# Kernel tuning notes

Measured on AMD Instinct MI355X. Metric: run time of the kernel, lower is better.

The kernel has to match this reference:

```python
import jax, jax.numpy as jnp
import numpy as np

D_MODEL = 768; D_REF = 768; N_LAYER = 8
EXPAND = 2; D_STATE = 128; HEADDIM = 64; D_CONV = 4
D_INNER = EXPAND * D_MODEL              # 1536
NHEADS = D_INNER // HEADDIM             # 24
CONV_DIM = D_INNER + 2 * D_STATE        # 1792
D_IN_PROJ = 2 * D_INNER + 2 * D_STATE + NHEADS  # 3352
AH = 8; AD = 64; AINNER = AH * AD       # cross-attn heads/dim
RMS_EPS = 1e-5; LN_EPS = 1e-6


def silu(x):
    return x * jax.nn.sigmoid(x)


def rmsnorm(x, w, eps=RMS_EPS):
    x = x.astype(jnp.float32)
    return x * jax.lax.rsqrt(jnp.mean(x * x, axis=-1, keepdims=True) + eps) * w


def ln_noaffine(x, eps=LN_EPS):
    m = jnp.mean(x, -1, keepdims=True)
    v = jnp.mean((x - m) ** 2, -1, keepdims=True)
    return (x - m) * jax.lax.rsqrt(v + eps)


def mamba2_mixer(u, in_w, conv_w, conv_b, dt_bias, A_log, D_ssm, nrm_w, out_w, out_b):
    Bsz, L, _ = u.shape
    zxbcdt = u @ in_w                                        # (B,L,3352)
    z = zxbcdt[..., :D_INNER]
    xBC = zxbcdt[..., D_INNER:D_INNER + CONV_DIM]
    dt = jax.nn.softplus(zxbcdt[..., D_INNER + CONV_DIM:] + dt_bias)  # (B,L,H)
    # causal depthwise conv over sequence + SiLU
    xt = jnp.transpose(xBC, (0, 2, 1))                       # (B,C,L)
    xt = jax.lax.conv_general_dilated(xt, conv_w[:, None, :], (1,), [(D_CONV - 1, 0)],
                                      feature_group_count=CONV_DIM)
    xBC = silu(jnp.transpose(xt, (0, 2, 1)) + conv_b)
    x = xBC[..., :D_INNER].reshape(Bsz, L, NHEADS, HEADDIM)
    Bm = xBC[..., D_INNER:D_INNER + D_STATE]                 # (B,L,N)
    Cm = xBC[..., D_INNER + D_STATE:]                        # (B,L,N)
    dA = jnp.exp(dt * (-jnp.exp(A_log)))                     # (B,L,H)

    def step(h, inp):
        dA_t, dt_t, x_t, B_t, C_t = inp
        dBx = jnp.einsum('bh,bhp,bn->bhpn', dt_t, x_t, B_t)
        h = h * dA_t[:, :, None, None] + dBx                 # (B,H,P,N)
        y = jnp.einsum('bhpn,bn->bhp', h, C_t)
        return h, y

    h0 = jnp.zeros((Bsz, NHEADS, HEADDIM, D_STATE), u.dtype)
    xs = (jnp.moveaxis(dA, 1, 0), jnp.moveaxis(dt, 1, 0), jnp.moveaxis(x, 1, 0),
          jnp.moveaxis(Bm, 1, 0), jnp.moveaxis(Cm, 1, 0))
    _, ys = jax.lax.scan(step, h0, xs)
    y = jnp.moveaxis(ys, 0, 1) + x * D_ssm[None, None, :, None]
    y = y.reshape(Bsz, L, D_INNER)
    y = rmsnorm(y * silu(z), nrm_w)                          # gated RMSNorm (norm_before_gate=False)
    return y @ out_w + out_b


def cross_attention(x, c, q_w, k_w, v_w, o_w, o_b):
    B, L, _ = x.shape
    q = (x @ q_w).reshape(B, L, AH, AD)
    k = (c @ k_w).reshape(B, -1, AH, AD)
    v = (c @ v_w).reshape(B, -1, AH, AD)
    a = jax.nn.softmax(jnp.einsum('blhd,bmhd->bhlm', q, k) * (AD ** -0.5), axis=-1)
    o = jnp.einsum('bhlm,bmhd->blhd', a, v).reshape(B, L, AINNER)
    return o @ o_w + o_b


def block_fwd(hidden, residual, cond, p):
    residual = hidden + residual
    hidden = rmsnorm(residual, p['norm_w'])
    aff = silu(jnp.mean(cond, axis=1)) @ p['ada_w'] + p['ada_b']
    sh_mba, sc_mba, g_mba, sh_msa, sc_msa, g_msa = jnp.split(aff, 6, axis=-1)
    mod = lambda t, sh, sc: t * (1 + sc[:, None, :]) + sh[:, None, :]
    hidden = hidden + g_mba[:, None, :] * mamba2_mixer(
        mod(hidden, sh_mba, sc_mba), p['in_w'], p['conv_w'], p['conv_b'],
        p['dt_bias'], p['A_log'], p['D_ssm'], p['ssm_norm_w'], p['out_w'], p['out_b'])
    hidden = hidden + g_msa[:, None, :] * cross_attention(
        mod(ln_noaffine(hidden), sh_msa, sc_msa), cond,
        p['q_w'], p['k_w'], p['v_w'], p['o_w'], p['o_b'])
    return hidden, residual


def backbone(hidden_states, ref_embeddings, norm_w, ada_w, ada_b, in_w, conv_w, conv_b,
             dt_bias, A_log, D_ssm, ssm_norm_w, out_w, out_b,
             q_w, k_w, v_w, o_w, o_b, norm_f_w):
    params = dict(norm_w=norm_w, ada_w=ada_w, ada_b=ada_b, in_w=in_w, conv_w=conv_w,
                  conv_b=conv_b, dt_bias=dt_bias, A_log=A_log, D_ssm=D_ssm,
                  ssm_norm_w=ssm_norm_w, out_w=out_w, out_b=out_b,
                  q_w=q_w, k_w=k_w, v_w=v_w, o_w=o_w, o_b=o_b)

    @jax.checkpoint
    def body(carry, lp):
        h, r = carry
        h, r = block_fwd(h, r, ref_embeddings, lp)
        return (h, r), None

    carry0 = (hidden_states, jnp.zeros_like(hidden_states))
    (h, r), _ = jax.lax.scan(body, carry0, params)
    return rmsnorm(h + r, norm_f_w)


def setup_inputs() -> dict:
    key = jax.random.key(0)
    ks = jax.random.split(key, 16)
    B, L, LC = 2, 512, 64

    def w(k, shape, s=0.02):
        return jax.random.normal(k, shape, jnp.float32) * s

    return dict(
        hidden_states=jax.random.normal(ks[0], (B, L, D_MODEL), jnp.float32),
        ref_embeddings=jax.random.normal(ks[1], (B, LC, D_REF), jnp.float32),
        norm_w=jnp.ones((N_LAYER, D_MODEL), jnp.float32),
        ada_w=w(ks[2], (N_LAYER, D_REF, 6 * D_MODEL)),
        ada_b=jnp.zeros((N_LAYER, 6 * D_MODEL), jnp.float32),
        in_w=w(ks[3], (N_LAYER, D_MODEL, D_IN_PROJ)),
        conv_w=w(ks[4], (N_LAYER, CONV_DIM, D_CONV), 0.2),
        conv_b=jnp.zeros((N_LAYER, CONV_DIM), jnp.float32),
        dt_bias=jnp.log(jnp.expm1(jax.random.uniform(ks[5], (N_LAYER, NHEADS), jnp.float32, 1e-3, 0.1))),
        A_log=jnp.log(jax.random.uniform(ks[6], (N_LAYER, NHEADS), jnp.float32, 1.0, 16.0)),
        D_ssm=jnp.ones((N_LAYER, NHEADS), jnp.float32),
        ssm_norm_w=jnp.ones((N_LAYER, D_INNER), jnp.float32),
        out_w=w(ks[7], (N_LAYER, D_INNER, D_MODEL)),
        out_b=jnp.zeros((N_LAYER, D_MODEL), jnp.float32),
        q_w=w(ks[8], (N_LAYER, D_MODEL, AINNER)),
        k_w=w(ks[9], (N_LAYER, D_REF, AINNER)),
        v_w=w(ks[10], (N_LAYER, D_REF, AINNER)),
        o_w=w(ks[11], (N_LAYER, AINNER, D_MODEL)),
        o_b=jnp.zeros((N_LAYER, D_MODEL), jnp.float32),
        norm_f_w=jnp.ones((D_MODEL,), jnp.float32),
    )


def reference(hidden_states, ref_embeddings, norm_w, ada_w, ada_b, in_w, conv_w, conv_b,
              dt_bias, A_log, D_ssm, ssm_norm_w, out_w, out_b,
              q_w, k_w, v_w, o_w, o_b, norm_f_w):
    return backbone(hidden_states, ref_embeddings, norm_w, ada_w, ada_b, in_w, conv_w,
                    conv_b, dt_bias, A_log, D_ssm, ssm_norm_w, out_w, out_b,
                    q_w, k_w, v_w, o_w, o_b, norm_f_w)
```

## Files before the change

kernel.cpp:

```cpp
#include <hip/hip_runtime.h>
#include <hip/hip_bf16.h>
#include <math.h>

#define D_MODEL   768
#define N_LAYER   8
#define D_INNER   1536
#define D_STATE   128
#define HEADDIM   64
#define NHEADS    24
#define CONV_DIM  1792
#define D_IN_PROJ 3352
#define AH        8
#define AD        64
#define AINNER    512
#define BSZ       2
#define SEQ       512
#define LC        64
#define ROWS      (BSZ*SEQ)
#define NCHUNK    8
#define CT        64
#define NP1       3456
#define AFF       4608

typedef __attribute__((ext_vector_type(8))) short bf16x8;
typedef __attribute__((ext_vector_type(4))) float f32x4;

__device__ __forceinline__ float siluf(float x) { return x / (1.f + expf(-x)); }

__device__ __forceinline__ unsigned short f2b(float x) {
    __hip_bfloat16 h = __float2bfloat16(x);
    return __builtin_bit_cast(unsigned short, h);
}
__device__ __forceinline__ float b2f(unsigned short u) {
    unsigned v = ((unsigned)u) << 16;
    return __builtin_bit_cast(float, v);
}

__device__ __forceinline__ void gload16(const void* g, void* l) {
    __builtin_amdgcn_global_load_lds(
        (const __attribute__((address_space(1))) unsigned int*)g,
        (__attribute__((address_space(3))) unsigned int*)l,
        16, 0, 0);
}

__device__ __forceinline__ float block_sum_256(float v, float* s4) {
    #pragma unroll
    for (int o = 32; o > 0; o >>= 1) v += __shfl_down(v, o, 64);
    __syncthreads();
    if ((threadIdx.x & 63) == 0) s4[threadIdx.x >> 6] = v;
    __syncthreads();
    return s4[0] + s4[1] + s4[2] + s4[3];
}

__global__ void k_prep(const float* __restrict__ ref_emb, unsigned short* __restrict__ ref_bf,
                       float* __restrict__ smc, const float* __restrict__ adab,
                       float* __restrict__ aff_all,
                       const float* __restrict__ in_w, const float* __restrict__ out_w,
                       const float* __restrict__ qw, const float* __restrict__ kw,
                       const float* __restrict__ vw, const float* __restrict__ ow,
                       unsigned short* __restrict__ in_wt, unsigned short* __restrict__ out_wt,
                       unsigned short* __restrict__ qwt, unsigned short* __restrict__ kwt,
                       unsigned short* __restrict__ vwt, unsigned short* __restrict__ owt) {
    int blk = blockIdx.x, t = threadIdx.x;
    if (blk < 384) {
        int i = blk * 256 + t;
        ref_bf[i] = f2b(ref_emb[i]);
        return;
    }
    if (blk < 390) {
        int i = (blk - 384) * 256 + t;
        if (i < BSZ * D_MODEL) {
            int b = i / D_MODEL, d = i % D_MODEL;
            const float* p = ref_emb + (size_t)b * LC * D_MODEL + d;
            float s = 0.f;
            #pragma unroll 4
            for (int l = 0; l < LC; l++) s += p[l * D_MODEL];
            smc[i] = siluf(s * (1.f / (float)LC));
        }
        return;
    }
    if (blk < 678) {
        int i = (blk - 390) * 256 + t;
        int j = i % AFF; int l = (i / AFF) >> 1;
        aff_all[i] = adab[l * AFF + j];
        return;
    }
    const float* src; unsigned short* dst; int K, N, n0, k0;
    if (blk < 21414) {
        int u = blk - 678; int z = u / 2592; int rem = u % 2592;
        k0 = (rem / 108) * 32; n0 = (rem % 108) * 32;
        src = in_w + (size_t)z * 768 * 3352; dst = in_wt + (size_t)z * 3456 * 768;
        K = 768; N = 3352;
    } else if (blk < 30630) {
        int u = blk - 21414; int z = u / 1152; int rem = u % 1152;
        k0 = (rem / 24) * 32; n0 = (rem % 24) * 32;
        src = out_w + (size_t)z * 1536 * 768; dst = out_wt + (size_t)z * 768 * 1536;
        K = 1536; N = 768;
    } else if (blk < 39846) {
        int u = blk - 30630; int z = u / 384; int rem = u % 384;
        k0 = (rem / 16) * 32; n0 = (rem % 16) * 32;
        int which = z >> 3, layer = z & 7;
        src = (which == 0 ? qw : which == 1 ? kw : vw) + (size_t)layer * 768 * 512;
        dst = (which == 0 ? qwt : which == 1 ? kwt : vwt) + (size_t)layer * 512 * 768;
        K = 768; N = 512;
    } else {
        int u = blk - 39846; int z = u / 384; int rem = u % 384;
        k0 = (rem / 24) * 32; n0 = (rem % 24) * 32;
        src = ow + (size_t)z * 512 * 768; dst = owt + (size_t)z * 768 * 512;
        K = 512; N = 768;
    }
    __shared__ float tile[32][33];
    int nl = t & 31, kl = t >> 5;
    #pragma unroll
    for (int p = 0; p < 4; p++) {
        int k = kl + p * 8;
        int n = n0 + nl;
        tile[k][nl] = (n < N) ? src[(size_t)(k0 + k) * N + n] : 0.f;
    }
    __syncthreads();
    int kl2 = t & 31, nl2 = t >> 5;
    #pragma unroll
    for (int p = 0; p < 4; p++) {
        int n = nl2 + p * 8;
        dst[(size_t)(n0 + n) * K + k0 + kl2] = f2b(tile[kl2][n]);
    }
}

__global__ __launch_bounds__(256)
void k_kvada(const unsigned short* __restrict__ A, const unsigned short* __restrict__ Kwt,
             const unsigned short* __restrict__ Vwt, unsigned short* __restrict__ Kb,
             unsigned short* __restrict__ Vb,
             const float* __restrict__ smc, const float* __restrict__ adaw,
             float* __restrict__ aff_all) {
    int z = blockIdx.z;
    if (z >= 16) {
        int zz = z - 16; int l = zz >> 3, kc = zz & 7;
        int j = blockIdx.x * 256 + threadIdx.x;
        const float* w = adaw + (size_t)l * D_MODEL * AFF + j;
        const float* x0 = smc;
        const float* x1 = smc + D_MODEL;
        float s0 = 0.f, s1 = 0.f;
        int d0 = kc * 96;
        #pragma unroll 8
        for (int d = d0; d < d0 + 96; d++) {
            float wv = w[(size_t)d * AFF];
            s0 += x0[d] * wv; s1 += x1[d] * wv;
        }
        atomicAdd(&aff_all[(size_t)l * BSZ * AFF + j], s0);
        atomicAdd(&aff_all[(size_t)l * BSZ * AFF + AFF + j], s1);
        return;
    }
    if (blockIdx.x >= 4) return;
    int layer = z >> 1; int which = z & 1;
    const unsigned short* Bt = (which ? Vwt : Kwt) + (size_t)layer * AINNER * D_MODEL;
    unsigned short* C = (which ? Vb : Kb) + (size_t)layer * (BSZ * LC) * AINNER;
    __shared__ __align__(16) unsigned short As[128][32];
    __shared__ __align__(16) unsigned short Bs[128][32];
    int n0 = blockIdx.x * 128;
    int tid = threadIdx.x;
    int lane = tid & 63, wave = tid >> 6;
    int wm = (wave >> 1) * 64, wn = (wave & 1) * 64;
    int l15 = lane & 15, quad = lane >> 4;
    f32x4 acc[4][4];
    #pragma unroll
    for (int i = 0; i < 4; i++)
        #pragma unroll
        for (int j = 0; j < 4; j++) acc[i][j] = (f32x4){0.f, 0.f, 0.f, 0.f};
    int srow = tid >> 2, schunk = (tid & 3) * 8;
    for (int k0 = 0; k0 < D_MODEL; k0 += 32) {
        #pragma unroll
        for (int ps = 0; ps < 2; ps++) {
            int r = srow + ps * 64;
            gload16(&A[(size_t)r * D_MODEL + k0 + schunk], &As[r][schunk]);
            gload16(&Bt[(size_t)(n0 + r) * D_MODEL + k0 + schunk], &Bs[r][schunk]);
        }
        __syncthreads();
        bf16x8 af[4], bfr[4];
        #pragma unroll
        for (int i = 0; i < 4; i++) af[i]  = *(const bf16x8*)&As[wm + i * 16 + l15][quad * 8];
        #pragma unroll
        for (int j = 0; j < 4; j++) bfr[j] = *(const bf16x8*)&Bs[wn + j * 16 + l15][quad * 8];
        #pragma unroll
        for (int i = 0; i < 4; i++)
            #pragma unroll
            for (int j = 0; j < 4; j++)
                acc[i][j] = __builtin_amdgcn_mfma_f32_16x16x32_bf16(af[i], bfr[j], acc[i][j], 0, 0, 0);
        __syncthreads();
    }
    #pragma unroll
    for (int i = 0; i < 4; i++) {
        #pragma unroll
        for (int j = 0; j < 4; j++) {
            int col = n0 + wn + j * 16 + l15;
            #pragma unroll
            for (int r = 0; r < 4; r++) {
                int row = wm + i * 16 + quad * 4 + r;
                C[(size_t)row * AINNER + col] = f2b(acc[i][j][r]);
            }
        }
    }
}

__global__ __launch_bounds__(256)
void k_gemm_sk(const unsigned short* __restrict__ A, const unsigned short* __restrict__ Bt,
               float* __restrict__ C, int M, int N, int K, int Kc) {
    int z = blockIdx.z;
    C += (size_t)z * M * N;
    int kbeg = z * Kc;
    int kend = kbeg + Kc; if (kend > K) kend = K;
    __shared__ __align__(16) unsigned short As[128][32];
    __shared__ __align__(16) unsigned short Bs[128][32];
    int m0 = blockIdx.y * 128, n0 = blockIdx.x * 128;
    int tid = threadIdx.x;
    int lane = tid & 63, wave = tid >> 6;
    int wm = (wave >> 1) * 64, wn = (wave & 1) * 64;
    int l15 = lane & 15, quad = lane >> 4;
    f32x4 acc[4][4];
    #pragma unroll
    for (int i = 0; i < 4; i++)
        #pragma unroll
        for (int j = 0; j < 4; j++) acc[i][j] = (f32x4){0.f, 0.f, 0.f, 0.f};

    int srow = tid >> 2;
    int schunk = (tid & 3) * 8;

    for (int k0 = kbeg; k0 < kend; k0 += 32) {
        #pragma unroll
        for (int ps = 0; ps < 2; ps++) {
            int r = srow + ps * 64;
            gload16(&A[(size_t)(m0 + r) * K + k0 + schunk], &As[r][schunk]);
            gload16(&Bt[(size_t)(n0 + r) * K + k0 + schunk], &Bs[r][schunk]);
        }
        __syncthreads();
        bf16x8 af[4], bfr[4];
        #pragma unroll
        for (int i = 0; i < 4; i++) af[i]  = *(const bf16x8*)&As[wm + i * 16 + l15][quad * 8];
        #pragma unroll
        for (int j = 0; j < 4; j++) bfr[j] = *(const bf16x8*)&Bs[wn + j * 16 + l15][quad * 8];
        #pragma unroll
        for (int i = 0; i < 4; i++)
            #pragma unroll
            for (int j = 0; j < 4; j++)
                acc[i][j] = __builtin_amdgcn_mfma_f32_16x16x32_bf16(af[i], bfr[j], acc[i][j], 0, 0, 0);
        __syncthreads();
    }
    #pragma unroll
    for (int i = 0; i < 4; i++) {
        #pragma unroll
        for (int j = 0; j < 4; j++) {
            int col = n0 + wn + j * 16 + l15;
            if (col < N) {
                #pragma unroll
                for (int r = 0; r < 4; r++) {
                    int row = m0 + wm + i * 16 + quad * 4 + r;
                    C[(size_t)row * N + col] = acc[i][j][r];
                }
            }
        }
    }
}

__global__ void k_addrmsmod(const float* __restrict__ hin, const float* __restrict__ raw,
                            const float* __restrict__ bias, const float* __restrict__ affprev,
                            float* __restrict__ residual, const float* __restrict__ normw,
                            const float* __restrict__ affcur,
                            float* __restrict__ hidden_n, unsigned short* __restrict__ u,
                            int has_raw) {
    __shared__ float s4[4];
    const size_t PSTR = (size_t)ROWS * D_MODEL;
    int row = blockIdx.x;
    int b = row >> 9;
    const float* hp = hin + (size_t)row * D_MODEL;
    float* rp = residual + (size_t)row * D_MODEL;
    float v[3]; float ss = 0.f;
    #pragma unroll
    for (int j = 0; j < 3; j++) {
        int d = threadIdx.x + j * 256;
        float x = hp[d];
        if (has_raw) {
            float g = affprev[b * AFF + 3840 + d];
            float rawv = raw[(size_t)row * D_MODEL + d] + raw[PSTR + (size_t)row * D_MODEL + d];
            x += g * (rawv + bias[d]) + rp[d];
        }
        rp[d] = x; v[j] = x; ss += x * x;
    }
    ss = block_sum_256(ss, s4);
    float inv = rsqrtf(ss / (float)D_MODEL + 1e-5f);
    const float* sh = affcur + b * AFF;
    const float* sc = affcur + b * AFF + 768;
    #pragma unroll
    for (int j = 0; j < 3; j++) {
        int d = threadIdx.x + j * 256;
        float hn = v[j] * inv * normw[d];
        hidden_n[(size_t)row * D_MODEL + d] = hn;
        u[(size_t)row * D_MODEL + d] = f2b(hn * (1.f + sc[d]) + sh[d]);
    }
}

__global__ void k_convdt(const float* __restrict__ zx, const float* __restrict__ convw,
                         const float* __restrict__ convb, const float* __restrict__ dtbias,
                         unsigned short* __restrict__ xBC, float* __restrict__ dtb) {
    const size_t PSTRZ = (size_t)ROWS * D_IN_PROJ;
    int i = blockIdx.x * 256 + threadIdx.x;
    if (i < ROWS * NHEADS) {
        int h = i % NHEADS; int row = i / NHEADS;
        size_t off = (size_t)row * D_IN_PROJ + D_INNER + CONV_DIM + h;
        float x = zx[off] + zx[off + PSTRZ] + dtbias[h];
        dtb[i] = (x > 20.f) ? x : log1pf(expf(x));
    }
    if (i >= ROWS * CONV_DIM) return;
    int c = i % CONV_DIM; int row = i / CONV_DIM;
    int l = row & 511; int b = row >> 9;
    float acc = convb[c];
    #pragma unroll
    for (int k = 0; k < 4; k++) {
        int t = l - 3 + k;
        if (t >= 0) {
            size_t idx = (size_t)(b * SEQ + t) * D_IN_PROJ + D_INNER + c;
            acc += convw[c * 4 + k] * (zx[idx] + zx[idx + PSTRZ]);
        }
    }
    xBC[i] = f2b(siluf(acc));
}

__global__ __launch_bounds__(256)
void k_ssm_par(const unsigned short* __restrict__ xBC, const float* __restrict__ dtb,
               const float* __restrict__ Alog, const float* __restrict__ Dssm,
               float* __restrict__ y, unsigned short* __restrict__ Sbuf,
               float* __restrict__ Pbuf) {
    __shared__ unsigned short sB[64][136];
    __shared__ unsigned short sC[64][136];
    __shared__ unsigned short sXT[64][72];
    __shared__ unsigned short sG[64][72];
    __shared__ unsigned short sBT[128][72];
    __shared__ float sL[64], sDt[64];
    int c = blockIdx.x, bh = blockIdx.y;
    int h = bh % NHEADS, b = bh / NHEADS;
    int tid = threadIdx.x;
    int lane = tid & 63, wave = tid >> 6;
    int l15 = lane & 15, quad = lane >> 4;
    int r = tid >> 2, q4 = tid & 3;
    int base = b * SEQ + c * CT;
    float a_h = expf(Alog[h]);
    float Dh = Dssm[h];
    if (tid < 64) {
        float dt = dtb[(base + tid) * NHEADS + h];
        float v = -a_h * dt;
        #pragma unroll
        for (int off = 1; off < 64; off <<= 1) {
            float u2 = __shfl_up(v, off, 64);
            if (tid >= off) v += u2;
        }
        sL[tid] = v; sDt[tid] = dt;
    }
    const unsigned short* xrow = xBC + (size_t)(base + r) * CONV_DIM;
    #pragma unroll
    for (int j = 0; j < 4; j++) {
        int n0 = q4 * 32 + j * 8;
        uint4 v = *(const uint4*)&xrow[D_INNER + n0];
        *(uint4*)&sB[r][n0] = v;
        const unsigned short* hv = (const unsigned short*)&v;
        #pragma unroll
        for (int e = 0; e < 8; e++) sBT[n0 + e][r] = hv[e];
        uint4 w = *(const uint4*)&xrow[D_INNER + D_STATE + n0];
        *(uint4*)&sC[r][n0] = w;
    }
    #pragma unroll
    for (int j = 0; j < 2; j++) {
        int p0 = q4 * 16 + j * 8;
        uint4 v = *(const uint4*)&xrow[h * HEADDIM + p0];
        const unsigned short* hv = (const unsigned short*)&v;
        #pragma unroll
        for (int e = 0; e < 8; e++) sXT[p0 + e][r] = hv[e];
    }
    __syncthreads();
    if (tid == 0) Pbuf[bh * NCHUNK + c] = expf(sL[63]);

    f32x4 acc1[4];
    #pragma unroll
    for (int j = 0; j < 4; j++) acc1[j] = (f32x4){0.f, 0.f, 0.f, 0.f};
    #pragma unroll
    for (int k0 = 0; k0 < 4; k0++) {
        bf16x8 a = *(const bf16x8*)&sC[wave * 16 + l15][k0 * 32 + quad * 8];
        #pragma unroll
        for (int nt = 0; nt < 4; nt++) {
            bf16x8 bv = *(const bf16x8*)&sB[nt * 16 + l15][k0 * 32 + quad * 8];
            acc1[nt] = __builtin_amdgcn_mfma_f32_16x16x32_bf16(a, bv, acc1[nt], 0, 0, 0);
        }
    }
    #pragma unroll
    for (int nt = 0; nt < 4; nt++) {
        int s = nt * 16 + l15;
        float Ls = sL[s], dts = sDt[s];
        #pragma unroll
        for (int rr = 0; rr < 4; rr++) {
            int i = wave * 16 + quad * 4 + rr;
            float g = (s <= i) ? acc1[nt][rr] * expf(sL[i] - Ls) * dts : 0.f;
            sG[i][s] = f2b(g);
        }
    }
    __syncthreads();

    f32x4 acc2[4];
    #pragma unroll
    for (int j = 0; j < 4; j++) acc2[j] = (f32x4){0.f, 0.f, 0.f, 0.f};
    #pragma unroll
    for (int k0 = 0; k0 < 2; k0++) {
        bf16x8 a = *(const bf16x8*)&sG[wave * 16 + l15][k0 * 32 + quad * 8];
        #pragma unroll
        for (int nt = 0; nt < 4; nt++) {
            bf16x8 bv = *(const bf16x8*)&sXT[nt * 16 + l15][k0 * 32 + quad * 8];
            acc2[nt] = __builtin_amdgcn_mfma_f32_16x16x32_bf16(a, bv, acc2[nt], 0, 0, 0);
        }
    }
    #pragma unroll
    for (int nt = 0; nt < 4; nt++) {
        int p = nt * 16 + l15;
        #pragma unroll
        for (int rr = 0; rr < 4; rr++) {
            int i = wave * 16 + quad * 4 + rr;
            float xv = b2f(sXT[p][i]);
            y[(size_t)(base + i) * D_INNER + h * HEADDIM + p] = acc2[nt][rr] + Dh * xv;
        }
    }
    __syncthreads();
    {
        float wr2 = expf(sL[63] - sL[r]) * sDt[r];
        #pragma unroll
        for (int j = 0; j < 16; j++) {
            int pp = q4 * 16 + j;
            sG[pp][r] = f2b(b2f(sXT[pp][r]) * wr2);
        }
    }
    __syncthreads();
    f32x4 accS[8];
    #pragma unroll
    for (int j = 0; j < 8; j++) accS[j] = (f32x4){0.f, 0.f, 0.f, 0.f};
    #pragma unroll
    for (int k0 = 0; k0 < 2; k0++) {
        bf16x8 a = *(const bf16x8*)&sG[wave * 16 + l15][k0 * 32 + quad * 8];
        #pragma unroll
        for (int nt = 0; nt < 8; nt++) {
            bf16x8 bv = *(const bf16x8*)&sBT[nt * 16 + l15][k0 * 32 + quad * 8];
            accS[nt] = __builtin_amdgcn_mfma_f32_16x16x32_bf16(a, bv, accS[nt], 0, 0, 0);
        }
    }
    unsigned short* sout = Sbuf + ((size_t)bh * NCHUNK + c) * 8192;
    #pragma unroll
    for (int nt = 0; nt < 8; nt++) {
        int n = nt * 16 + l15;
        #pragma unroll
        for (int rr = 0; rr < 4; rr++) {
            int p = wave * 16 + quad * 4 + rr;
            sout[p * 128 + n] = f2b(accS[nt][rr]);
        }
    }
}

__global__ __launch_bounds__(256)
void k_ssm_fix(const unsigned short* __restrict__ xBC, const float* __restrict__ dtb,
               const float* __restrict__ Alog, const unsigned short* __restrict__ Sbuf,
               const float* __restrict__ Pbuf, float* __restrict__ y) {
    __shared__ unsigned short sC[64][136];
    __shared__ unsigned short sHB[64][136];
    __shared__ float sL[64];
    int c = blockIdx.x + 1, bh = blockIdx.y;
    int h = bh % NHEADS, b = bh / NHEADS;
    int tid = threadIdx.x;
    int lane = tid & 63, wave = tid >> 6;
    int l15 = lane & 15, quad = lane >> 4;
    int r = tid >> 2, q4 = tid & 3;
    int base = b * SEQ + c * CT;
    if (tid < 64) {
        float dt = dtb[(base + tid) * NHEADS + h];
        float v = -expf(Alog[h]) * dt;
        #pragma unroll
        for (int off = 1; off < 64; off <<= 1) {
            float u2 = __shfl_up(v, off, 64);
            if (tid >= off) v += u2;
        }
        sL[tid] = v;
    }
    float hacc[32];
    #pragma unroll
    for (int e = 0; e < 32; e++) hacc[e] = 0.f;
    {
        const unsigned short* sp = Sbuf + (size_t)bh * NCHUNK * 8192 + r * 128 + q4 * 32;
        float w = 1.f;
        for (int j = c - 1; j >= 0; j--) {
            const unsigned short* srow = sp + (size_t)j * 8192;
            #pragma unroll
            for (int q = 0; q < 4; q++) {
                bf16x8 vv = *(const bf16x8*)&srow[q * 8];
                #pragma unroll
                for (int e = 0; e < 8; e++)
                    hacc[q * 8 + e] += w * b2f((unsigned short)vv[e]);
            }
            w *= Pbuf[bh * NCHUNK + j];
        }
    }
    __syncthreads();
    #pragma unroll
    for (int e = 0; e < 32; e++) sHB[r][q4 * 32 + e] = f2b(hacc[e]);
    {
        float el = expf(sL[r]);
        const unsigned short* xrow = xBC + (size_t)(base + r) * CONV_DIM + D_INNER + D_STATE;
        #pragma unroll
        for (int j = 0; j < 4; j++) {
            int n0 = q4 * 32 + j * 8;
            uint4 v = *(const uint4*)&xrow[n0];
            const unsigned short* hv = (const unsigned short*)&v;
            #pragma unroll
            for (int e = 0; e < 8; e++) sC[r][n0 + e] = f2b(b2f(hv[e]) * el);
        }
    }
    __syncthreads();
    f32x4 acc[4];
    #pragma unroll
    for (int j = 0; j < 4; j++) acc[j] = (f32x4){0.f, 0.f, 0.f, 0.f};
    #pragma unroll
    for (int k0 = 0; k0 < 4; k0++) {
        bf16x8 a = *(const bf16x8*)&sC[wave * 16 + l15][k0 * 32 + quad * 8];
        #pragma unroll
        for (int nt = 0; nt < 4; nt++) {
            bf16x8 bv = *(const bf16x8*)&sHB[nt * 16 + l15][k0 * 32 + quad * 8];
            acc[nt] = __builtin_amdgcn_mfma_f32_16x16x32_bf16(a, bv, acc[nt], 0, 0, 0);
        }
    }
    #pragma unroll
    for (int nt = 0; nt < 4; nt++) {
        int p = nt * 16 + l15;
        #pragma unroll
        for (int rr = 0; rr < 4; rr++) {
            int i = wave * 16 + quad * 4 + rr;
            size_t idx = (size_t)(base + i) * D_INNER + h * HEADDIM + p;
            y[idx] += acc[nt][rr];
        }
    }
}

__global__ void k_gatednorm(const float* __restrict__ yscan, const float* __restrict__ zx,
                            const float* __restrict__ nw, unsigned short* __restrict__ out) {
    __shared__ float s4[4];
    const size_t PSTRZ = (size_t)ROWS * D_IN_PROJ;
    int row = blockIdx.x;
    const float* yp = yscan + (size_t)row * D_INNER;
    const float* zp0 = zx + (size_t)row * D_IN_PROJ;
    const float* zp1 = zp0 + PSTRZ;
    float v[6]; float ss = 0.f;
    #pragma unroll
    for (int j = 0; j < 6; j++) {
        int d = threadIdx.x + j * 256;
        float val = yp[d] * siluf(zp0[d] + zp1[d]);
        v[j] = val; ss += val * val;
    }
    ss = block_sum_256(ss, s4);
    float inv = rsqrtf(ss / (float)D_INNER + 1e-5f);
    #pragma unroll
    for (int j = 0; j < 6; j++) {
        int d = threadIdx.x + j * 256;
        out[(size_t)row * D_INNER + d] = f2b(v[j] * inv * nw[d]);
    }
}

__global__ void k_fuse_ln(const float* __restrict__ hidden_n, const float* __restrict__ tmp,
                          const float* __restrict__ outb, const float* __restrict__ aff,
                          float* __restrict__ hidden2, unsigned short* __restrict__ attnx) {
    __shared__ float s4[4];
    const size_t PSTR = (size_t)ROWS * D_MODEL;
    int row = blockIdx.x;
    int b = row >> 9;
    const float* gm = aff + b * AFF + 1536;
    float v[3]; float s = 0.f;
    #pragma unroll
    for (int j = 0; j < 3; j++) {
        int d = threadIdx.x + j * 256;
        size_t idx = (size_t)row * D_MODEL + d;
        float t = tmp[idx] + tmp[idx + PSTR] + tmp[idx + 2 * PSTR] + tmp[idx + 3 * PSTR];
        float x = hidden_n[idx] + gm[d] * (t + outb[d]);
        hidden2[idx] = x;
        v[j] = x; s += x;
    }
    float mean = block_sum_256(s, s4) / (float)D_MODEL;
    float ss = 0.f;
    #pragma unroll
    for (int j = 0; j < 3; j++) { float c = v[j] - mean; ss += c * c; }
    float var = block_sum_256(ss, s4) / (float)D_MODEL;
    float inv = rsqrtf(var + 1e-6f);
    const float* sh = aff + b * AFF + 2304;
    const float* sc = aff + b * AFF + 3072;
    #pragma unroll
    for (int j = 0; j < 3; j++) {
        int d = threadIdx.x + j * 256;
        float xh = (v[j] - mean) * inv;
        attnx[(size_t)row * D_MODEL + d] = f2b(xh * (1.f + sc[d]) + sh[d]);
    }
}

__global__ __launch_bounds__(256)
void k_attn(const unsigned short* __restrict__ attnx, const unsigned short* __restrict__ qwt,
            const unsigned short* __restrict__ kb, const unsigned short* __restrict__ vb,
            unsigned short* __restrict__ ob) {
    int blk = blockIdx.x;
    int lt = blk & 15; int h = (blk >> 4) & 7; int b = blk >> 7;
    __shared__ unsigned short sK[64][72];
    __shared__ unsigned short sVT[64][72];
    __shared__ unsigned short sA[32][136];
    __shared__ unsigned short sW[64][136];
    __shared__ unsigned short sQb[32][72];
    __shared__ unsigned short sP[32][72];
    int tid = threadIdx.x;
    {
        int r = tid >> 2, c0 = (tid & 3) * 16;
        const unsigned short* kp = kb + (size_t)(b * LC + r) * AINNER + h * AD + c0;
        const unsigned short* vp = vb + (size_t)(b * LC + r) * AINNER + h * AD + c0;
        #pragma unroll
        for (int j = 0; j < 4; j++) {
            *(ushort4*)&sK[r][c0 + j * 4] = *(const ushort4*)&kp[j * 4];
            ushort4 vv = *(const ushort4*)&vp[j * 4];
            const unsigned short* hv = (const unsigned short*)&vv;
            #pragma unroll
            for (int e = 0; e < 4; e++) sVT[c0 + j * 4 + e][r] = hv[e];
        }
    }
    int lane = tid & 63, wave = tid >> 6;
    int l15 = lane & 15, quad = lane >> 4;
    int rt = wave >> 1, cp = (wave & 1) * 2;
    f32x4 accq[2];
    accq[0] = (f32x4){0.f, 0.f, 0.f, 0.f};
    accq[1] = (f32x4){0.f, 0.f, 0.f, 0.f};
    const size_t arow_base = (size_t)(b * SEQ + lt * 32) * D_MODEL;
    for (int k0 = 0; k0 < D_MODEL; k0 += 128) {
        __syncthreads();
        #pragma unroll
        for (int j = 0; j < 2; j++) {
            int s = tid + j * 256; int row = s >> 4, c8 = (s & 15) * 8;
            *(uint4*)&sA[row][c8] =
                *(const uint4*)&attnx[arow_base + (size_t)row * D_MODEL + k0 + c8];
        }
        #pragma unroll
        for (int j = 0; j < 4; j++) {
            int s = tid + j * 256; int row = s >> 4, c8 = (s & 15) * 8;
            *(uint4*)&sW[row][c8] =
                *(const uint4*)&qwt[(size_t)(h * AD + row) * D_MODEL + k0 + c8];
        }
        __syncthreads();
        #pragma unroll
        for (int ks = 0; ks < 4; ks++) {
            bf16x8 af = *(const bf16x8*)&sA[rt * 16 + l15][ks * 32 + quad * 8];
            #pragma unroll
            for (int j = 0; j < 2; j++) {
                bf16x8 bf = *(const bf16x8*)&sW[(cp + j) * 16 + l15][ks * 32 + quad * 8];
                accq[j] = __builtin_amdgcn_mfma_f32_16x16x32_bf16(af, bf, accq[j], 0, 0, 0);
            }
        }
    }
    #pragma unroll
    for (int j = 0; j < 2; j++)
        #pragma unroll
        for (int rr = 0; rr < 4; rr++)
            sQb[rt * 16 + quad * 4 + rr][(cp + j) * 16 + l15] = f2b(accq[j][rr] * 0.125f);
    __syncthreads();
    if (wave < 2) {
        int qt = wave;
        f32x4 s[4];
        #pragma unroll
        for (int mt = 0; mt < 4; mt++) s[mt] = (f32x4){0.f, 0.f, 0.f, 0.f};
        #pragma unroll
        for (int k0 = 0; k0 < 2; k0++) {
            bf16x8 aq = *(const bf16x8*)&sQb[qt * 16 + l15][k0 * 32 + quad * 8];
            #pragma unroll
            for (int mt = 0; mt < 4; mt++) {
                bf16x8 bk = *(const bf16x8*)&sK[mt * 16 + l15][k0 * 32 + quad * 8];
                s[mt] = __builtin_amdgcn_mfma_f32_16x16x32_bf16(aq, bk, s[mt], 0, 0, 0);
            }
        }
        #pragma unroll
        for (int rr = 0; rr < 4; rr++) {
            float mx = fmaxf(fmaxf(s[0][rr], s[1][rr]), fmaxf(s[2][rr], s[3][rr]));
            #pragma unroll
            for (int off = 8; off > 0; off >>= 1) mx = fmaxf(mx, __shfl_xor(mx, off, 64));
            float e0 = expf(s[0][rr] - mx), e1 = expf(s[1][rr] - mx);
            float e2 = expf(s[2][rr] - mx), e3 = expf(s[3][rr] - mx);
            float sum = e0 + e1 + e2 + e3;
            #pragma unroll
            for (int off = 8; off > 0; off >>= 1) sum += __shfl_xor(sum, off, 64);
            float inv = 1.f / sum;
            int q = qt * 16 + quad * 4 + rr;
            sP[q][0 * 16 + l15] = f2b(e0 * inv);
            sP[q][1 * 16 + l15] = f2b(e1 * inv);
            sP[q][2 * 16 + l15] = f2b(e2 * inv);
            sP[q][3 * 16 + l15] = f2b(e3 * inv);
        }
    }
    __syncthreads();
    {
        int qt = wave >> 1, dp = (wave & 1) * 2;
        f32x4 o[2];
        o[0] = (f32x4){0.f, 0.f, 0.f, 0.f};
        o[1] = (f32x4){0.f, 0.f, 0.f, 0.f};
        #pragma unroll
        for (int k0 = 0; k0 < 2; k0++) {
            bf16x8 ap = *(const bf16x8*)&sP[qt * 16 + l15][k0 * 32 + quad * 8];
            #pragma unroll
            for (int j = 0; j < 2; j++) {
                bf16x8 bv = *(const bf16x8*)&sVT[(dp + j) * 16 + l15][k0 * 32 + quad * 8];
                o[j] = __builtin_amdgcn_mfma_f32_16x16x32_bf16(ap, bv, o[j], 0, 0, 0);
            }
        }
        #pragma unroll
        for (int j = 0; j < 2; j++) {
            int d = (dp + j) * 16 + l15;
            #pragma unroll
            for (int rr = 0; rr < 4; rr++) {
                int q = qt * 16 + quad * 4 + rr;
                ob[(size_t)(b * SEQ + lt * 32 + q) * AINNER + h * AD + d] = f2b(o[j][rr]);
            }
        }
    }
}

__global__ void k_final(const float* __restrict__ hidden2, const float* __restrict__ raw,
                        const float* __restrict__ bias, const float* __restrict__ aff,
                        const float* __restrict__ residual, const float* __restrict__ w,
                        float* __restrict__ out) {
    __shared__ float s4[4];
    const size_t PSTR = (size_t)ROWS * D_MODEL;
    int row = blockIdx.x;
    int b = row >> 9;
    const float* gm = aff + b * AFF + 3840;
    float v[3]; float ss = 0.f;
    #pragma unroll
    for (int j = 0; j < 3; j++) {
        int d = threadIdx.x + j * 256;
        size_t idx = (size_t)row * D_MODEL + d;
        float rawv = raw[idx] + raw[idx + PSTR];
        float x = hidden2[idx] + gm[d] * (rawv + bias[d]) + residual[idx];
        v[j] = x; ss += x * x;
    }
    ss = block_sum_256(ss, s4);
    float inv = rsqrtf(ss / (float)D_MODEL + 1e-5f);
    #pragma unroll
    for (int j = 0; j < 3; j++) {
        int d = threadIdx.x + j * 256;
        out[(size_t)row * D_MODEL + d] = v[j] * inv * w[d];
    }
}

extern "C" void kernel_launch(void* const* d_in, const int* in_sizes, int n_in,
                              void* d_out, int out_size, void* d_ws, size_t ws_size,
                              hipStream_t stream) {
    const float* hidden_states = (const float*)d_in[0];
    const float* ref_emb  = (const float*)d_in[1];
    const float* norm_w   = (const float*)d_in[2];
    const float* ada_w    = (const float*)d_in[3];
    const float* ada_b    = (const float*)d_in[4];
    const float* in_w     = (const float*)d_in[5];
    const float* conv_w   = (const float*)d_in[6];
    const float* conv_b   = (const float*)d_in[7];
    const float* dt_bias  = (const float*)d_in[8];
    const float* A_log    = (const float*)d_in[9];
    const float* D_ssm    = (const float*)d_in[10];
    const float* ssm_nw   = (const float*)d_in[11];
    const float* out_w    = (const float*)d_in[12];
    const float* out_b    = (const float*)d_in[13];
    const float* q_w      = (const float*)d_in[14];
    const float* k_w      = (const float*)d_in[15];
    const float* v_w      = (const float*)d_in[16];
    const float* o_w      = (const float*)d_in[17];
    const float* o_b      = (const float*)d_in[18];
    const float* norm_f_w = (const float*)d_in[19];
    float* out = (float*)d_out;

    char* p = (char*)d_ws;
    auto alloc = [&](size_t bytes) -> char* {
        char* r = p; p += (bytes + 255) & ~(size_t)255; return r;
    };
    float* residual = (float*)alloc((size_t)ROWS * D_MODEL * 4);
    float* hidden2  = (float*)alloc((size_t)ROWS * D_MODEL * 4);
    float* hidden_n = (float*)alloc((size_t)ROWS * D_MODEL * 4);
    float* tmpM     = (float*)alloc((size_t)4 * ROWS * D_MODEL * 4);
    float* tmpO     = (float*)alloc((size_t)2 * ROWS * D_MODEL * 4);
    float* zx       = (float*)alloc((size_t)2 * ROWS * D_IN_PROJ * 4);
    float* dtb      = (float*)alloc((size_t)ROWS * NHEADS * 4);
    float* yscan    = (float*)alloc((size_t)ROWS * D_INNER * 4);
    float* aff_all  = (float*)alloc((size_t)N_LAYER * BSZ * AFF * 4);
    float* smc      = (float*)alloc((size_t)BSZ * D_MODEL * 4);
    float* Pbuf     = (float*)alloc((size_t)BSZ * NHEADS * NCHUNK * 4);
    unsigned short* xBC    = (unsigned short*)alloc((size_t)ROWS * CONV_DIM * 2);
    unsigned short* Sbuf   = (unsigned short*)alloc((size_t)BSZ * NHEADS * NCHUNK * 8192 * 2);
    unsigned short* u_bf   = (unsigned short*)alloc((size_t)ROWS * D_MODEL * 2);
    unsigned short* ynorm  = (unsigned short*)alloc((size_t)ROWS * D_INNER * 2);
    unsigned short* attnx  = (unsigned short*)alloc((size_t)ROWS * D_MODEL * 2);
    unsigned short* ob     = (unsigned short*)alloc((size_t)ROWS * AINNER * 2);
    unsigned short* ref_bf = (unsigned short*)alloc((size_t)BSZ * LC * D_MODEL * 2);
    unsigned short* kb_all  = (unsigned short*)alloc((size_t)N_LAYER * BSZ * LC * AINNER * 2);
    unsigned short* vb_all  = (unsigned short*)alloc((size_t)N_LAYER * BSZ * LC * AINNER * 2);
    unsigned short* in_wt_all  = (unsigned short*)alloc((size_t)N_LAYER * NP1 * D_MODEL * 2);
    unsigned short* out_wt_all = (unsigned short*)alloc((size_t)N_LAYER * D_MODEL * D_INNER * 2);
    unsigned short* q_wt_all   = (unsigned short*)alloc((size_t)N_LAYER * AINNER * D_MODEL * 2);
    unsigned short* o_wt_all   = (unsigned short*)alloc((size_t)N_LAYER * D_MODEL * AINNER * 2);
    unsigned short* kwt_all = (unsigned short*)alloc((size_t)N_LAYER * AINNER * D_MODEL * 2);
    unsigned short* vwt_all = (unsigned short*)alloc((size_t)N_LAYER * AINNER * D_MODEL * 2);

    k_prep<<<42918, 256, 0, stream>>>(ref_emb, ref_bf, smc, ada_b, aff_all,
                                      in_w, out_w, q_w, k_w, v_w, o_w,
                                      in_wt_all, out_wt_all, q_wt_all, kwt_all, vwt_all,
                                      o_wt_all);
    k_kvada<<<dim3(18, 1, 80), 256, 0, stream>>>(ref_bf, kwt_all, vwt_all, kb_all, vb_all,
                                                 smc, ada_w, aff_all);

    for (int layer = 0; layer < N_LAYER; layer++) {
        const float* L_norm_w  = norm_w  + layer * D_MODEL;
        const float* L_conv_w  = conv_w  + layer * CONV_DIM * 4;
        const float* L_conv_b  = conv_b  + layer * CONV_DIM;
        const float* L_dt_bias = dt_bias + layer * NHEADS;
        const float* L_A_log   = A_log   + layer * NHEADS;
        const float* L_D_ssm   = D_ssm   + layer * NHEADS;
        const float* L_ssm_nw  = ssm_nw  + layer * D_INNER;
        const float* L_out_b   = out_b   + layer * D_MODEL;
        const float* L_o_b_prev= o_b     + (layer - 1) * D_MODEL;
        const float* L_aff     = aff_all + (size_t)layer * BSZ * AFF;
        const float* L_aff_prev= aff_all + (size_t)(layer - 1) * BSZ * AFF;
        const unsigned short* in_wt  = in_wt_all  + (size_t)layer * NP1 * D_MODEL;
        const unsigned short* out_wt = out_wt_all + (size_t)layer * D_MODEL * D_INNER;
        const unsigned short* q_wt   = q_wt_all   + (size_t)layer * AINNER * D_MODEL;
        const unsigned short* o_wt   = o_wt_all   + (size_t)layer * D_MODEL * AINNER;

        k_addrmsmod<<<ROWS, 256, 0, stream>>>(
            layer == 0 ? hidden_states : hidden2, tmpO,
            layer == 0 ? o_b : L_o_b_prev,
            layer == 0 ? aff_all : L_aff_prev,
            residual, L_norm_w, L_aff, hidden_n, u_bf, layer == 0 ? 0 : 1);
        k_gemm_sk<<<dim3(NP1 / 128, ROWS / 128, 2), 256, 0, stream>>>(u_bf, in_wt, zx, ROWS, D_IN_PROJ, D_MODEL, 384);
        k_convdt<<<(ROWS * CONV_DIM + 255) / 256, 256, 0, stream>>>(zx, L_conv_w, L_conv_b, L_dt_bias, xBC, dtb);
        k_ssm_par<<<dim3(NCHUNK, BSZ * NHEADS), 256, 0, stream>>>(xBC, dtb, L_A_log, L_D_ssm, yscan, Sbuf, Pbuf);
        k_ssm_fix<<<dim3(NCHUNK - 1, BSZ * NHEADS), 256, 0, stream>>>(xBC, dtb, L_A_log, Sbuf, Pbuf, yscan);
        k_gatednorm<<<ROWS, 256, 0, stream>>>(yscan, zx, L_ssm_nw, ynorm);
        k_gemm_sk<<<dim3(D_MODEL / 128, ROWS / 128, 4), 256, 0, stream>>>(ynorm, out_wt, tmpM, ROWS, D_MODEL, D_INNER, 384);
        k_fuse_ln<<<ROWS, 256, 0, stream>>>(hidden_n, tmpM, L_out_b, L_aff, hidden2, attnx);
        k_attn<<<BSZ * AH * 16, 256, 0, stream>>>(
            attnx, q_wt,
            kb_all + (size_t)layer * BSZ * LC * AINNER,
            vb_all + (size_t)layer * BSZ * LC * AINNER, ob);
        k_gemm_sk<<<dim3(D_MODEL / 128, ROWS / 128, 2), 256, 0, stream>>>(ob, o_wt, tmpO, ROWS, D_MODEL, AINNER, 256);
    }
    k_final<<<ROWS, 256, 0, stream>>>(hidden2, tmpO, o_b + (N_LAYER - 1) * D_MODEL,
                                      aff_all + (size_t)(N_LAYER - 1) * BSZ * AFF,
                                      residual, norm_f_w, out);
}
```

Before: 1.139 ms.

## Vectorize weight transpose prep with 64x64 tiles and double-buffer split-K GEMM

Weight conversion and transpose in the prep kernel now use 64x64 tiles with float4 loads and ushort4 stores, and the ref_emb cast is vectorized. This cuts the block count and the number of memory transactions in a large one-time preprocessing pass. The split-K GEMM gains a double-buffered LDS stage that prefetches the next K tile before computing the current one, using explicit vmcnt waits and raw barriers. That doubles LDS use and relies on gload16 issuing exactly four outstanding loads per stage for the vmcnt(4) wait to be correct.

```diff
diff --git a/kernel.cpp b/kernel.cpp
--- a/kernel.cpp
+++ b/kernel.cpp
@@ -62,13 +62,15 @@
                        unsigned short* __restrict__ qwt, unsigned short* __restrict__ kwt,
                        unsigned short* __restrict__ vwt, unsigned short* __restrict__ owt) {
     int blk = blockIdx.x, t = threadIdx.x;
-    if (blk < 384) {
-        int i = blk * 256 + t;
-        ref_bf[i] = f2b(ref_emb[i]);
+    if (blk < 96) {
+        int i4 = blk * 256 + t;
+        float4 v = *(const float4*)&ref_emb[(size_t)i4 * 4];
+        ushort4 o; o.x = f2b(v.x); o.y = f2b(v.y); o.z = f2b(v.z); o.w = f2b(v.w);
+        *(ushort4*)&ref_bf[(size_t)i4 * 4] = o;
         return;
     }
-    if (blk < 390) {
-        int i = (blk - 384) * 256 + t;
+    if (blk < 102) {
+        int i = (blk - 96) * 256 + t;
         if (i < BSZ * D_MODEL) {
             int b = i / D_MODEL, d = i % D_MODEL;
             const float* p = ref_emb + (size_t)b * LC * D_MODEL + d;
@@ -79,50 +81,57 @@
         }
         return;
     }
-    if (blk < 678) {
-        int i = (blk - 390) * 256 + t;
+    if (blk < 390) {
+        int i = (blk - 102) * 256 + t;
         int j = i % AFF; int l = (i / AFF) >> 1;
         aff_all[i] = adab[l * AFF + j];
         return;
     }
     const float* src; unsigned short* dst; int K, N, n0, k0;
-    if (blk < 21414) {
-        int u = blk - 678; int z = u / 2592; int rem = u % 2592;
-        k0 = (rem / 108) * 32; n0 = (rem % 108) * 32;
+    int u = blk - 390;
+    if (u < 5184) {
+        int z = u / 648, rem = u % 648;
+        k0 = (rem / 54) * 64; n0 = (rem % 54) * 64;
         src = in_w + (size_t)z * 768 * 3352; dst = in_wt + (size_t)z * 3456 * 768;
         K = 768; N = 3352;
-    } else if (blk < 30630) {
-        int u = blk - 21414; int z = u / 1152; int rem = u % 1152;
-        k0 = (rem / 24) * 32; n0 = (rem % 24) * 32;
+    } else if (u < 7488) {
+        u -= 5184; int z = u / 288, rem = u % 288;
+        k0 = (rem / 12) * 64; n0 = (rem % 12) * 64;
         src = out_w + (size_t)z * 1536 * 768; dst = out_wt + (size_t)z * 768 * 1536;
         K = 1536; N = 768;
-    } else if (blk < 39846) {
-        int u = blk - 30630; int z = u / 384; int rem = u % 384;
-        k0 = (rem / 16) * 32; n0 = (rem % 16) * 32;
+    } else if (u < 9792) {
+        u -= 7488; int z = u / 96, rem = u % 96;
+        k0 = (rem / 8) * 64; n0 = (rem % 8) * 64;
         int which = z >> 3, layer = z & 7;
         src = (which == 0 ? qw : which == 1 ? kw : vw) + (size_t)layer * 768 * 512;
         dst = (which == 0 ? qwt : which == 1 ? kwt : vwt) + (size_t)layer * 512 * 768;
         K = 768; N = 512;
     } else {
-        int u = blk - 39846; int z = u / 384; int rem = u % 384;
-        k0 = (rem / 24) * 32; n0 = (rem % 24) * 32;
+        u -= 9792; int z = u / 96, rem = u % 96;
+        k0 = (rem / 12) * 64; n0 = (rem % 12) * 64;
         src = ow + (size_t)z * 512 * 768; dst = owt + (size_t)z * 768 * 512;
         K = 512; N = 768;
     }
-    __shared__ float tile[32][33];
-    int nl = t & 31, kl = t >> 5;
-    #pragma unroll
-    for (int p = 0; p < 4; p++) {
-        int k = kl + p * 8;
-        int n = n0 + nl;
-        tile[k][nl] = (n < N) ? src[(size_t)(k0 + k) * N + n] : 0.f;
-    }
-    __syncthreads();
-    int kl2 = t & 31, nl2 = t >> 5;
-    #pragma unroll
-    for (int p = 0; p < 4; p++) {
-        int n = nl2 + p * 8;
-        dst[(size_t)(n0 + n) * K + k0 + kl2] = f2b(tile[kl2][n]);
+    __shared__ float tile[64][65];
+    #pragma unroll
+    for (int p2 = 0; p2 < 4; p2++) {
+        int k = (t >> 4) + p2 * 16;
+        int c = (t & 15) * 4;
+        int n = n0 + c;
+        float4 v = (float4){0.f, 0.f, 0.f, 0.f};
+        if (n < N) v = *(const float4*)&src[(size_t)(k0 + k) * N + n];
+        tile[k][c + 0] = v.x; tile[k][c + 1] = v.y;
+        tile[k][c + 2] = v.z; tile[k][c + 3] = v.w;
+    }
+    __syncthreads();
+    #pragma unroll
+    for (int p2 = 0; p2 < 4; p2++) {
+        int n = (t >> 4) + p2 * 16;
+        int kk = (t & 15) * 4;
+        ushort4 o;
+        o.x = f2b(tile[kk + 0][n]); o.y = f2b(tile[kk + 1][n]);
+        o.z = f2b(tile[kk + 2][n]); o.w = f2b(tile[kk + 3][n]);
+        *(ushort4*)&dst[(size_t)(n0 + n) * K + k0 + kk] = o;
     }
 }
 
@@ -208,8 +217,9 @@
     C += (size_t)z * M * N;
     int kbeg = z * Kc;
     int kend = kbeg + Kc; if (kend > K) kend = K;
-    __shared__ __align__(16) unsigned short As[128][32];
-    __shared__ __align__(16) unsigned short Bs[128][32];
+    int nt = (kend - kbeg) >> 5;
+    __shared__ __align__(16) unsigned short As[2][128][32];
+    __shared__ __align__(16) unsigned short Bs[2][128][32];
     int m0 = blockIdx.y * 128, n0 = blockIdx.x * 128;
     int tid = threadIdx.x;
     int lane = tid & 63, wave = tid >> 6;
@@ -224,26 +234,40 @@
     int srow = tid >> 2;
     int schunk = (tid & 3) * 8;
 
-    for (int k0 = kbeg; k0 < kend; k0 += 32) {
-        #pragma unroll
-        for (int ps = 0; ps < 2; ps++) {
-            int r = srow + ps * 64;
-            gload16(&A[(size_t)(m0 + r) * K + k0 + schunk], &As[r][schunk]);
-            gload16(&Bt[(size_t)(n0 + r) * K + k0 + schunk], &Bs[r][schunk]);
-        }
-        __syncthreads();
+    #define STAGE_SK(buf, kk0)                                                        \
+        do {                                                                          \
+            _Pragma("unroll")                                                         \
+            for (int ps = 0; ps < 2; ps++) {                                          \
+                int r = srow + ps * 64;                                               \
+                gload16(&A[(size_t)(m0 + r) * K + (kk0) + schunk], &As[buf][r][schunk]); \
+                gload16(&Bt[(size_t)(n0 + r) * K + (kk0) + schunk], &Bs[buf][r][schunk]); \
+            }                                                                         \
+        } while (0)
+
+    STAGE_SK(0, kbeg);
+    int cur = 0;
+    for (int it = 0; it < nt; ++it) {
+        if (it + 1 < nt) {
+            STAGE_SK(cur ^ 1, kbeg + (it + 1) * 32);
+            asm volatile("s_waitcnt vmcnt(4)" ::: "memory");
+        } else {
+            asm volatile("s_waitcnt vmcnt(0)" ::: "memory");
+        }
+        __builtin_amdgcn_s_barrier();
         bf16x8 af[4], bfr[4];
         #pragma unroll
-        for (int i = 0; i < 4; i++) af[i]  = *(const bf16x8*)&As[wm + i * 16 + l15][quad * 8];
-        #pragma unroll
-        for (int j = 0; j < 4; j++) bfr[j] = *(const bf16x8*)&Bs[wn + j * 16 + l15][quad * 8];
+        for (int i = 0; i < 4; i++) af[i]  = *(const bf16x8*)&As[cur][wm + i * 16 + l15][quad * 8];
+        #pragma unroll
+        for (int j = 0; j < 4; j++) bfr[j] = *(const bf16x8*)&Bs[cur][wn + j * 16 + l15][quad * 8];
         #pragma unroll
         for (int i = 0; i < 4; i++)
             #pragma unroll
             for (int j = 0; j < 4; j++)
                 acc[i][j] = __builtin_amdgcn_mfma_f32_16x16x32_bf16(af[i], bfr[j], acc[i][j], 0, 0, 0);
-        __syncthreads();
-    }
+        __builtin_amdgcn_s_barrier();
+        cur ^= 1;
+    }
+    #undef STAGE_SK
     #pragma unroll
     for (int i = 0; i < 4; i++) {
         #pragma unroll
@@ -803,7 +827,7 @@
     unsigned short* kwt_all = (unsigned short*)alloc((size_t)N_LAYER * AINNER * D_MODEL * 2);
     unsigned short* vwt_all = (unsigned short*)alloc((size_t)N_LAYER * AINNER * D_MODEL * 2);
 
-    k_prep<<<42918, 256, 0, stream>>>(ref_emb, ref_bf, smc, ada_b, aff_all,
+    k_prep<<<10950, 256, 0, stream>>>(ref_emb, ref_bf, smc, ada_b, aff_all,
                                       in_w, out_w, q_w, k_w, v_w, o_w,
                                       in_wt_all, out_wt_all, q_wt_all, kwt_all, vwt_all,
                                       o_wt_all);
```

After: 1.089 ms. 4.4% less time.
